# Optimization experiments

Hardware: AMD Instinct MI355X
Metric: run time of the kernel (lower is better)

Reference implementation:

```python
import jax, jax.numpy as jnp
import numpy as np


def setup_inputs() -> dict:
    key = jax.random.key(0)
    k1, k2, k3, k4 = jax.random.split(key, 4)
    N, T, F = 8192, 128, 9
    M_s = 256
    merged = jax.random.normal(k1, (N, T, F), dtype=jnp.float32)
    input1 = jax.random.normal(k2, (N, T, F), dtype=jnp.float32)
    samples = jax.random.normal(k3, (N, M_s), dtype=jnp.float32)
    labels = jax.random.randint(k4, (N,), 0, 10, dtype=jnp.int32)
    return {"merged": merged, "input1": input1, "samples": samples, "labels": labels}


def reference(merged, input1, samples, labels):
    # Pairwise squared distances S_ij = sum_k (s_i - s_j)^2 / M_s, computed via
    # the Gram-matrix identity instead of materializing the [N, N, M_s] tensor.
    M_s = samples.shape[1]
    sq = jnp.sum(samples * samples, axis=-1)                 # [N]
    gram = jnp.einsum('im,jm->ij', samples, samples)         # [N, N]
    S_ij = (sq[:, None] + sq[None, :] - 2.0 * gram) / jnp.float32(M_s)
    same = (labels[:, None] == labels[None, :]).astype(jnp.float32)
    term2 = jnp.mean(jnp.maximum(0.0, (1.0 - same) * (1.0 - S_ij)))
    L_label = 10.0 * jnp.mean(same * S_ij) + 10.0 * term2
    return L_label
```

## Files before the change

### kernel.cpp

```cpp
#include <hip/hip_runtime.h>

#define NROWS 8192
#define KDIM  256
#define NT    64
#define NBLK  (NT * (NT + 1) / 2)
#define GRID  256

typedef __attribute__((ext_vector_type(4)))  float f32x4;
typedef __attribute__((ext_vector_type(16))) float f32x16;
typedef __attribute__((ext_vector_type(4)))  int   i32x4;
typedef __attribute__((ext_vector_type(8)))  int   i32x8;

#define GLD(gp, lp)                                                            \
  __builtin_amdgcn_global_load_lds(                                            \
      (const __attribute__((address_space(1))) void*)(gp),                     \
      (__attribute__((address_space(3))) void*)(lp), 16, 0, 0)

__global__ void prep_kernel(const float* __restrict__ samples,
                            const int* __restrict__ labels,
                            unsigned char* __restrict__ sf8,
                            float2* __restrict__ meta,
                            float* __restrict__ accg) {
  int row = blockIdx.x, t = threadIdx.x;
  float2 v2 = ((const float2*)samples)[(size_t)row * 128 + t];
  int pk = __builtin_amdgcn_cvt_pk_fp8_f32(v2.x, v2.y, 0, false);
  ((unsigned short*)sf8)[(size_t)row * 128 + t] = (unsigned short)(pk & 0xffff);
  float p = v2.x * v2.x + v2.y * v2.y;
#pragma unroll
  for (int off = 32; off; off >>= 1) p += __shfl_down(p, off);
  __shared__ float ws2[2];
  if ((t & 63) == 0) ws2[t >> 6] = p;
  __syncthreads();
  if (t == 0) {
    float tot = ws2[0] + ws2[1];
    meta[row] = make_float2(tot * (1.0f / 256.0f), (float)labels[row]);
  }
  if (row == 0 && t < 2) accg[t] = 0.0f;
}

__device__ inline void decode_tile(int b, int& bi, int& bj) {
  float disc = (2.0f * NT + 1.0f) * (2.0f * NT + 1.0f) - 8.0f * (float)b;
  bi = (int)(((2.0f * NT + 1.0f) - sqrtf(disc)) * 0.5f);
  if (bi < 0) bi = 0;
  if (bi > NT - 1) bi = NT - 1;
  while (bi > 0 && (bi * NT - bi * (bi - 1) / 2) > b) --bi;
  while (((bi + 1) * NT - (bi + 1) * bi / 2) <= b) ++bi;
  bj = bi + (b - (bi * NT - bi * (bi - 1) / 2));
}

__global__ __launch_bounds__(512, 1) void pair_kernel(
    const unsigned char* __restrict__ sf8, const float2* __restrict__ meta,
    float* __restrict__ accg) {

  __shared__ __align__(16) unsigned char As[2][128 * 256];
  __shared__ __align__(16) unsigned char Bs[2][128 * 256];
  __shared__ float red[8];

  int t = threadIdx.x;
  int lane = t & 63;
  int w = t >> 6;
  int wm = w >> 1, wn = w & 1;
  int lr = lane >> 4, pc = lane & 15;
  int l31 = lane & 31;
  int hk  = lane >> 5;

  float stt = 0.f;

  auto stage = [&](int bi_, int bj_, int buf) {
    int rA = bi_ * 128, rB = bj_ * 128;
#pragma unroll
    for (int p = 0; p < 4; ++p) {
      int region = p * 8 + w;
      int rr = region * 4 + lr;
      int c = pc ^ (rr & 15);
      GLD(sf8 + (size_t)(rA + rr) * KDIM + c * 16, &As[buf][region * 1024]);
      GLD(sf8 + (size_t)(rB + rr) * KDIM + c * 16, &Bs[buf][region * 1024]);
    }
  };

  int tile = blockIdx.x;
  int bi, bj;
  decode_tile(tile, bi, bj);
  stage(bi, bj, 0);
  int cur = 0;

  while (tile < NBLK) {
    int ntile = tile + GRID;
    int nbi = 0, nbj = 0;
    bool have_next = ntile < NBLK;
    if (have_next) decode_tile(ntile, nbi, nbj);

    __syncthreads();

    int rowA0 = bi * 128, rowB0 = bj * 128;
    float sqa_s[16], laaf[16];
#pragma unroll
    for (int g = 0; g < 4; ++g) {
      int gr = rowA0 + wm * 32 + g * 8 + 4 * hk;
      f32x4 m0 = *(const f32x4*)(meta + gr);
      f32x4 m1 = *(const f32x4*)(meta + gr + 2);
      sqa_s[g * 4 + 0] = m0.x; laaf[g * 4 + 0] = m0.y;
      sqa_s[g * 4 + 1] = m0.z; laaf[g * 4 + 1] = m0.w;
      sqa_s[g * 4 + 2] = m1.x; laaf[g * 4 + 2] = m1.y;
      sqa_s[g * 4 + 3] = m1.z; laaf[g * 4 + 3] = m1.w;
    }
    float sqb_s[2], labf[2];
#pragma unroll
    for (int j = 0; j < 2; ++j) {
      float2 mb = meta[rowB0 + wn * 64 + j * 32 + l31];
      sqb_s[j] = mb.x; labf[j] = mb.y;
    }

    if (have_next) stage(nbi, nbj, cur ^ 1);

    f32x16 acc[2];
#pragma unroll
    for (int j = 0; j < 2; ++j)
#pragma unroll
      for (int e = 0; e < 16; ++e) acc[j][e] = 0.f;

#pragma unroll
    for (int kt = 0; kt < 4; ++kt) {
      int c0 = kt * 4 + hk * 2;
      int m = wm * 32 + l31;
      const unsigned char* ab = &As[cur][m * 256];
      int sm = m & 15;
      i32x4 alo = *(const i32x4*)(ab + ((c0 ^ sm) << 4));
      i32x4 ahi = *(const i32x4*)(ab + (((c0 + 1) ^ sm) << 4));
      i32x8 av = {alo.x, alo.y, alo.z, alo.w, ahi.x, ahi.y, ahi.z, ahi.w};
#pragma unroll
      for (int j = 0; j < 2; ++j) {
        int n = wn * 64 + j * 32 + l31;
        const unsigned char* bb = &Bs[cur][n * 256];
        int sn = n & 15;
        i32x4 blo = *(const i32x4*)(bb + ((c0 ^ sn) << 4));
        i32x4 bhi = *(const i32x4*)(bb + (((c0 + 1) ^ sn) << 4));
        i32x8 bv = {blo.x, blo.y, blo.z, blo.w, bhi.x, bhi.y, bhi.z, bhi.w};
        acc[j] = __builtin_amdgcn_mfma_scale_f32_32x32x64_f8f6f4(
            av, bv, acc[j], 0, 0, 0, 127, 0, 127);
      }
    }

    float s = 0.f;
#pragma unroll
    for (int j = 0; j < 2; ++j) {
#pragma unroll
      for (int g2 = 0; g2 < 16; ++g2) {
        float S = sqa_s[g2] + sqb_s[j] - acc[j][g2] * (1.0f / 128.0f);
        float h = fmaxf(0.f, 1.f - S);
        s += (laaf[g2] == labf[j]) ? S : h;
      }
    }
    stt += ((bi == bj) ? 1.0f : 2.0f) * s;

    tile = ntile; bi = nbi; bj = nbj; cur ^= 1;
  }

#pragma unroll
  for (int off = 32; off; off >>= 1) stt += __shfl_down(stt, off);
  if (lane == 0) red[w] = stt;
  __syncthreads();
  if (t == 0) {
    float a = 0.f;
#pragma unroll
    for (int k = 0; k < 8; k++) a += red[k];
    atomicAdd(&accg[0], a);
  }
}

__global__ void finalize_kernel(const float* __restrict__ accg,
                                float* __restrict__ out) {
  out[0] = 10.0f * accg[0] * (1.0f / ((float)NROWS * (float)NROWS));
}

extern "C" void kernel_launch(void* const* d_in, const int* in_sizes, int n_in,
                              void* d_out, int out_size, void* d_ws,
                              size_t ws_size, hipStream_t stream) {
  const float* samples = (const float*)d_in[2];
  const int*   labels  = (const int*)d_in[3];

  char* ws = (char*)d_ws;
  unsigned char* sf8 = (unsigned char*)ws;
  float2* meta = (float2*)(ws + (size_t)NROWS * KDIM);
  float* accg  = (float*)(ws + (size_t)NROWS * KDIM + NROWS * 8);
  float* out   = (float*)d_out;

  prep_kernel<<<NROWS, 128, 0, stream>>>(samples, labels, sf8, meta, accg);
  pair_kernel<<<GRID, 512, 0, stream>>>(sf8, meta, accg);
  finalize_kernel<<<1, 1, 0, stream>>>(accg, out);
}
```

Baseline: 124.6 us.

## Software-pipeline MFMA and epilogue across tiles, drop finalize kernel

Double-buffers the MFMA accumulators so that each iteration issues the current tile's matrix multiplies and then runs the previous tile's distance and hinge epilogue, letting VALU work overlap with MFMA latency. Per-row metadata for the previous tile is reloaded just before its epilogue. Separately, the finalize kernel is removed: the output is zeroed in the prep kernel and each block atomically adds its pre-scaled partial sum, saving one launch. Holding two accumulator sets raises register pressure, and the scaled atomic accumulation changes float summation order slightly.

```diff
diff --git a/kernel.cpp b/kernel.cpp
--- a/kernel.cpp
+++ b/kernel.cpp
@@ -20,7 +20,7 @@
                             const int* __restrict__ labels,
                             unsigned char* __restrict__ sf8,
                             float2* __restrict__ meta,
-                            float* __restrict__ accg) {
+                            float* __restrict__ out) {
   int row = blockIdx.x, t = threadIdx.x;
   float2 v2 = ((const float2*)samples)[(size_t)row * 128 + t];
   int pk = __builtin_amdgcn_cvt_pk_fp8_f32(v2.x, v2.y, 0, false);
@@ -35,7 +35,7 @@
     float tot = ws2[0] + ws2[1];
     meta[row] = make_float2(tot * (1.0f / 256.0f), (float)labels[row]);
   }
-  if (row == 0 && t < 2) accg[t] = 0.0f;
+  if (row == 0 && t == 0) out[0] = 0.0f;
 }
 
 __device__ inline void decode_tile(int b, int& bi, int& bj) {
@@ -50,7 +50,7 @@
 
 __global__ __launch_bounds__(512, 1) void pair_kernel(
     const unsigned char* __restrict__ sf8, const float2* __restrict__ meta,
-    float* __restrict__ accg) {
+    float* __restrict__ out) {
 
   __shared__ __align__(16) unsigned char As[2][128 * 256];
   __shared__ __align__(16) unsigned char Bs[2][128 * 256];
@@ -84,41 +84,34 @@
   stage(bi, bj, 0);
   int cur = 0;
 
-  while (tile < NBLK) {
-    int ntile = tile + GRID;
-    int nbi = 0, nbj = 0;
-    bool have_next = ntile < NBLK;
-    if (have_next) decode_tile(ntile, nbi, nbj);
-
-    __syncthreads();
-
-    int rowA0 = bi * 128, rowB0 = bj * 128;
-    float sqa_s[16], laaf[16];
+  int pbi = 0, pbj = 0;
+  float sqa[16], laa[16], sqb[2], labv[2], pwt = 1.f;
+  f32x16 accA[2], accB[2];
+
+  auto load_scalars = [&](int pbi_, int pbj_) {
 #pragma unroll
     for (int g = 0; g < 4; ++g) {
-      int gr = rowA0 + wm * 32 + g * 8 + 4 * hk;
+      int gr = pbi_ * 128 + wm * 32 + g * 8 + 4 * hk;
       f32x4 m0 = *(const f32x4*)(meta + gr);
       f32x4 m1 = *(const f32x4*)(meta + gr + 2);
-      sqa_s[g * 4 + 0] = m0.x; laaf[g * 4 + 0] = m0.y;
-      sqa_s[g * 4 + 1] = m0.z; laaf[g * 4 + 1] = m0.w;
-      sqa_s[g * 4 + 2] = m1.x; laaf[g * 4 + 2] = m1.y;
-      sqa_s[g * 4 + 3] = m1.z; laaf[g * 4 + 3] = m1.w;
-    }
-    float sqb_s[2], labf[2];
+      sqa[g * 4 + 0] = m0.x; laa[g * 4 + 0] = m0.y;
+      sqa[g * 4 + 1] = m0.z; laa[g * 4 + 1] = m0.w;
+      sqa[g * 4 + 2] = m1.x; laa[g * 4 + 2] = m1.y;
+      sqa[g * 4 + 3] = m1.z; laa[g * 4 + 3] = m1.w;
+    }
 #pragma unroll
     for (int j = 0; j < 2; ++j) {
-      float2 mb = meta[rowB0 + wn * 64 + j * 32 + l31];
-      sqb_s[j] = mb.x; labf[j] = mb.y;
-    }
-
-    if (have_next) stage(nbi, nbj, cur ^ 1);
-
-    f32x16 acc[2];
+      float2 mb = meta[pbj_ * 128 + wn * 64 + j * 32 + l31];
+      sqb[j] = mb.x; labv[j] = mb.y;
+    }
+    pwt = (pbi_ == pbj_) ? 1.0f : 2.0f;
+  };
+
+  auto domfma = [&](f32x16 (&acc)[2]) {
 #pragma unroll
     for (int j = 0; j < 2; ++j)
 #pragma unroll
       for (int e = 0; e < 16; ++e) acc[j][e] = 0.f;
-
 #pragma unroll
     for (int kt = 0; kt < 4; ++kt) {
       int c0 = kt * 4 + hk * 2;
@@ -140,21 +133,51 @@
             av, bv, acc[j], 0, 0, 0, 127, 0, 127);
       }
     }
-
+  };
+
+  auto epi = [&](const f32x16 (&acc)[2]) {
     float s = 0.f;
 #pragma unroll
     for (int j = 0; j < 2; ++j) {
 #pragma unroll
       for (int g2 = 0; g2 < 16; ++g2) {
-        float S = sqa_s[g2] + sqb_s[j] - acc[j][g2] * (1.0f / 128.0f);
+        float S = sqa[g2] + sqb[j] - acc[j][g2] * (1.0f / 128.0f);
         float h = fmaxf(0.f, 1.f - S);
-        s += (laaf[g2] == labf[j]) ? S : h;
+        s += (laa[g2] == labv[j]) ? S : h;
       }
     }
-    stt += ((bi == bj) ? 1.0f : 2.0f) * s;
-
-    tile = ntile; bi = nbi; bj = nbj; cur ^= 1;
+    stt += pwt * s;
+  };
+
+  int k = 0;
+  while (tile < NBLK) {
+    int ntile = tile + GRID;
+    int nbi = 0, nbj = 0;
+    bool have_next = ntile < NBLK;
+    if (have_next) decode_tile(ntile, nbi, nbj);
+
+    __syncthreads();
+
+    bool have_prev = (k > 0);
+    if (have_prev) load_scalars(pbi, pbj);
+
+    if (have_next) stage(nbi, nbj, cur ^ 1);
+
+    if (k & 1) {
+      domfma(accB);
+      if (have_prev) epi(accA);
+    } else {
+      domfma(accA);
+      if (have_prev) epi(accB);
+    }
+
+    pbi = bi; pbj = bj;
+    tile = ntile; bi = nbi; bj = nbj; cur ^= 1; ++k;
   }
+
+  load_scalars(pbi, pbj);
+  if ((k - 1) & 1) epi(accB);
+  else             epi(accA);
 
 #pragma unroll
   for (int off = 32; off; off >>= 1) stt += __shfl_down(stt, off);
@@ -163,14 +186,9 @@
   if (t == 0) {
     float a = 0.f;
 #pragma unroll
-    for (int k = 0; k < 8; k++) a += red[k];
-    atomicAdd(&accg[0], a);
+    for (int q = 0; q < 8; q++) a += red[q];
+    atomicAdd(&out[0], a * (10.0f / ((float)NROWS * (float)NROWS)));
   }
-}
-
-__global__ void finalize_kernel(const float* __restrict__ accg,
-                                float* __restrict__ out) {
-  out[0] = 10.0f * accg[0] * (1.0f / ((float)NROWS * (float)NROWS));
 }
 
 extern "C" void kernel_launch(void* const* d_in, const int* in_sizes, int n_in,
@@ -182,10 +200,8 @@
   char* ws = (char*)d_ws;
   unsigned char* sf8 = (unsigned char*)ws;
   float2* meta = (float2*)(ws + (size_t)NROWS * KDIM);
-  float* accg  = (float*)(ws + (size_t)NROWS * KDIM + NROWS * 8);
   float* out   = (float*)d_out;
 
-  prep_kernel<<<NROWS, 128, 0, stream>>>(samples, labels, sf8, meta, accg);
-  pair_kernel<<<GRID, 512, 0, stream>>>(sf8, meta, accg);
-  finalize_kernel<<<1, 1, 0, stream>>>(accg, out);
-}
+  prep_kernel<<<NROWS, 128, 0, stream>>>(samples, labels, sf8, meta, out);
+  pair_kernel<<<GRID, 512, 0, stream>>>(sf8, meta, out);
+}
```

Result: no change. 123.1 us, median of 2 (-1.2%).
